# Kernel tuning notes

Measured on AMD Instinct MI355X. Metric: run time of the kernel, lower is better.

## Reference

```python
import jax, jax.numpy as jnp
import numpy as np

EPS = 1e-12


def agnn_layer(x, row, col, num_nodes):
    """AGNN propagation with beta frozen at 1.0 (requires_grad=False in source).
    alpha_ij = softmax_{j in N(i)} ( beta * cos(x_i, x_j) ); out_i = sum_j alpha_ij * x_j.
    row = destination node of each edge (segment id), col = source node.
    """
    xn = x / (jnp.linalg.norm(x, axis=-1, keepdims=True) + EPS)  # unit-norm features
    score = jnp.sum(xn[row] * xn[col], axis=-1)                   # [E] beta=1 * cos sim
    smax = jax.ops.segment_max(score, row, num_segments=num_nodes)
    e = jnp.exp(score - smax[row])                                # stable softmax numerator
    denom = jax.ops.segment_sum(e, row, num_segments=num_nodes)
    alpha = e / jnp.maximum(denom[row], EPS)                      # [E]
    out = jax.ops.segment_sum(alpha[:, None] * x[col], row, num_segments=num_nodes)
    return out


def setup_inputs() -> dict:
    key = jax.random.key(0)
    ks = jax.random.split(key, 8)
    N, E = 100000, 1600000
    IN_DIM, HID, OUT_DIM = 128, 64, 64
    x = jax.random.normal(ks[0], (N, IN_DIM), dtype=jnp.float32)
    edge_row = jnp.sort(jax.random.randint(ks[1], (E,), 0, N))
    edge_col = jax.random.randint(ks[2], (E,), 0, N)
    # Linear params (PyTorch nn.Linear style: y = x @ W.T + b)
    s1 = 1.0 / np.sqrt(IN_DIM)
    W1 = jax.random.uniform(ks[3], (HID, IN_DIM), jnp.float32, -s1, s1)
    b1 = jax.random.uniform(ks[4], (HID,), jnp.float32, -s1, s1)
    s2 = 1.0 / np.sqrt(HID)
    W2 = jax.random.uniform(ks[5], (OUT_DIM, HID), jnp.float32, -s2, s2)
    b2 = jax.random.uniform(ks[6], (OUT_DIM,), jnp.float32, -s2, s2)
    return {"x": x, "edge_row": edge_row, "edge_col": edge_col,
            "W1": W1, "b1": b1, "W2": W2, "b2": b2}


def reference(x, edge_row, edge_col, W1, b1, W2, b2):
    N = x.shape[0]
    h = jax.nn.relu(x @ W1.T + b1)
    for _ in range(4):  # 4 frozen-beta AGNN layers
        h = jax.nn.relu(agnn_layer(h, edge_row, edge_col, N))
    return h @ W2.T + b2
```

## Files before the change

### kernel.cpp

```cpp
#include <hip/hip_runtime.h>


typedef _Float16 h2 __attribute__((ext_vector_type(2)));

union U4H { uint4 u; h2 h[4]; };
union U2H { uint2 u; h2 h[2]; };
union UHI { unsigned u; h2 h; };

#define DEV_INLINE __device__ __forceinline__

DEV_INLINE h2 mkh2(float a, float b) {
    h2 r; r.x = (_Float16)a; r.y = (_Float16)b; return r;
}

__global__ __launch_bounds__(256) void build_rowptr_scan(const int* __restrict__ row,
                                                         int* __restrict__ ptr,
                                                         int N, int E) {
    int e = blockIdx.x * blockDim.x + threadIdx.x;
    if (e >= E) return;
    const int r1 = row[e];
    const int r0 = (e == 0) ? -1 : row[e - 1];
    for (int i = r0 + 1; i <= r1; ++i) ptr[i] = e;
    if (e == E - 1) {
        for (int i = r1 + 1; i <= N; ++i) ptr[i] = E;
    }
}

#define PSEG 1024
__global__ __launch_bounds__(1024) void build_perm_seg(const int* __restrict__ ptr,
                                                       int* __restrict__ perm,
                                                       int N) {
    __shared__ int hist[256];
    __shared__ int tmp[256];
    const int t    = threadIdx.x;
    const int base = blockIdx.x * PSEG;
    const int end  = (base + PSEG < N) ? base + PSEG : N;
    const int cnt  = end - base;

    if (t < 256) hist[t] = 0;
    __syncthreads();

    int d = -1;
    if (t < cnt) {
        d = ptr[base + t + 1] - ptr[base + t];
        if (d > 255) d = 255;
        atomicAdd(&hist[d], 1);
    }
    __syncthreads();

    int h0 = (t < 256) ? hist[t] : 0;
    int* src = hist; int* dst = tmp;
    for (int off = 1; off < 256; off <<= 1) {
        if (t < 256) dst[t] = src[t] + (t >= off ? src[t - off] : 0);
        __syncthreads();
        int* tt = src; src = dst; dst = tt;
    }
    if (t < 256) src[t] -= h0;
    __syncthreads();

    if (t < cnt) {
        int pos = base + atomicAdd(&src[d], 1);
        perm[pos] = base + t;
    }
}

__global__ __launch_bounds__(512) void gemm1_relu(const float* __restrict__ x,
                                                  const float* __restrict__ W1,
                                                  const float* __restrict__ b1,
                                                  unsigned short* __restrict__ xn,
                                                  float* __restrict__ nrm,
                                                  int N) {
    __shared__ __align__(16) float Wt[32 * 64];
    __shared__ __align__(16) float xT[32 * 128];
    const int tid  = threadIdx.x;
    const int tx   = tid & 15;
    const int ty   = tid >> 4;
    const int base = blockIdx.x * 128;

    const float4* W4  = (const float4*)W1;
    const float4* x4p = (const float4*)x;

    const int wO  = tid & 63;
    const int wK4 = tid >> 6;
    const int mA  = tid & 127;
    const int kA  = tid >> 7;
    const int mB  = mA;
    const int kB  = kA + 4;
    const int nodeA = base + mA;

    float4 wv, xa_, xb_;
    wv = W4[wO * 32 + wK4];
    xa_ = make_float4(0.f, 0.f, 0.f, 0.f);
    xb_ = xa_;
    if (nodeA < N) {
        xa_ = x4p[(size_t)nodeA * 32 + kA];
        xb_ = x4p[(size_t)nodeA * 32 + kB];
    }

    float4 b4 = ((const float4*)b1)[tx];
    float4 acc[4];
    acc[0] = b4; acc[1] = b4; acc[2] = b4; acc[3] = b4;

    for (int c = 0; c < 4; ++c) {
        Wt[(4 * wK4 + 0) * 64 + wO] = wv.x;
        Wt[(4 * wK4 + 1) * 64 + wO] = wv.y;
        Wt[(4 * wK4 + 2) * 64 + wO] = wv.z;
        Wt[(4 * wK4 + 3) * 64 + wO] = wv.w;
        xT[(4 * kA + 0) * 128 + mA] = xa_.x;
        xT[(4 * kA + 1) * 128 + mA] = xa_.y;
        xT[(4 * kA + 2) * 128 + mA] = xa_.z;
        xT[(4 * kA + 3) * 128 + mA] = xa_.w;
        xT[(4 * kB + 0) * 128 + mB] = xb_.x;
        xT[(4 * kB + 1) * 128 + mB] = xb_.y;
        xT[(4 * kB + 2) * 128 + mB] = xb_.z;
        xT[(4 * kB + 3) * 128 + mB] = xb_.w;
        __syncthreads();

        if (c < 3) {
            const int ko = (c + 1) * 8;
            wv = W4[wO * 32 + ko + wK4];
            if (nodeA < N) {
                xa_ = x4p[(size_t)nodeA * 32 + ko + kA];
                xb_ = x4p[(size_t)nodeA * 32 + ko + kB];
            }
        }

#pragma unroll 4
        for (int k = 0; k < 32; ++k) {
            const float4 w4 = *(const float4*)&Wt[k * 64 + 4 * tx];
            const float4 xv = *(const float4*)&xT[k * 128 + 4 * ty];
            acc[0].x = fmaf(xv.x, w4.x, acc[0].x);
            acc[0].y = fmaf(xv.x, w4.y, acc[0].y);
            acc[0].z = fmaf(xv.x, w4.z, acc[0].z);
            acc[0].w = fmaf(xv.x, w4.w, acc[0].w);
            acc[1].x = fmaf(xv.y, w4.x, acc[1].x);
            acc[1].y = fmaf(xv.y, w4.y, acc[1].y);
            acc[1].z = fmaf(xv.y, w4.z, acc[1].z);
            acc[1].w = fmaf(xv.y, w4.w, acc[1].w);
            acc[2].x = fmaf(xv.z, w4.x, acc[2].x);
            acc[2].y = fmaf(xv.z, w4.y, acc[2].y);
            acc[2].z = fmaf(xv.z, w4.z, acc[2].z);
            acc[2].w = fmaf(xv.z, w4.w, acc[2].w);
            acc[3].x = fmaf(xv.w, w4.x, acc[3].x);
            acc[3].y = fmaf(xv.w, w4.y, acc[3].y);
            acc[3].z = fmaf(xv.w, w4.z, acc[3].z);
            acc[3].w = fmaf(xv.w, w4.w, acc[3].w);
        }
        if (c < 3) __syncthreads();
    }

#pragma unroll
    for (int mm = 0; mm < 4; ++mm) {
        float4 r = acc[mm];
        r.x = fmaxf(r.x, 0.f); r.y = fmaxf(r.y, 0.f);
        r.z = fmaxf(r.z, 0.f); r.w = fmaxf(r.w, 0.f);
        float s = fmaf(r.x, r.x, fmaf(r.y, r.y, fmaf(r.z, r.z, r.w * r.w)));
        s += __shfl_xor(s, 1, 64);
        s += __shfl_xor(s, 2, 64);
        s += __shfl_xor(s, 4, 64);
        s += __shfl_xor(s, 8, 64);
        const float nn  = sqrtf(s) + 1e-12f;
        const float inv = 1.f / nn;
        int node = base + 4 * ty + mm;
        if (node < N) {
            U2H pk;
            pk.h[0] = mkh2(r.x * inv, r.y * inv);
            pk.h[1] = mkh2(r.z * inv, r.w * inv);
            *(uint2*)&xn[(size_t)node * 64 + 4 * tx] = pk.u;
            if (tx == mm) nrm[node] = nn;
        }
    }
}

__global__ __launch_bounds__(256) void agnn_layer(const uint4* __restrict__ xn4,
                                                  const float* __restrict__ nrm,
                                                  const int* __restrict__ ptr,
                                                  const int* __restrict__ col,
                                                  const int* __restrict__ perm,
                                                  uint4* __restrict__ xo4,
                                                  float* __restrict__ nrmo,
                                                  int N) {
    const int tid  = threadIdx.x;
    const int lane = tid & 63;
    const int g    = (lane >> 3) & 1;
    const int sub  = lane & 7;
    const int slot = blockIdx.x * 16 + (tid >> 4);
    if (slot >= N) return;
    const int i = perm[slot];

    U4H hi_;
    hi_.u = xn4[(unsigned)i * 8u + sub];
    {
        const _Float16 L2E = (_Float16)1.4426950408889634f;
        h2 l2 = {L2E, L2E};
#pragma unroll
        for (int t = 0; t < 4; ++t) hi_.h[t] *= l2;
    }

    const int p0 = ptr[i], p1 = ptr[i + 1];

    float den = 0.f;
    U4H acc;
    acc.h[0] = mkh2(0.f, 0.f); acc.h[1] = mkh2(0.f, 0.f);
    acc.h[2] = mkh2(0.f, 0.f); acc.h[3] = mkh2(0.f, 0.f);

#define EDGE_BODY(VU, NRMJ)                                                  \
    {                                                                        \
        U4H xa; xa.u = (VU);                                                 \
        float s = 0.f;                                                       \
        s = __builtin_amdgcn_fdot2(hi_.h[0], xa.h[0], s, false);             \
        s = __builtin_amdgcn_fdot2(hi_.h[1], xa.h[1], s, false);             \
        s = __builtin_amdgcn_fdot2(hi_.h[2], xa.h[2], s, false);             \
        s = __builtin_amdgcn_fdot2(hi_.h[3], xa.h[3], s, false);             \
        s += __shfl_xor(s, 1, 64);                                           \
        s += __shfl_xor(s, 2, 64);                                           \
        s += __shfl_xor(s, 4, 64);                                           \
        const float p = exp2f(s);                                            \
        den += p;                                                            \
        const _Float16 wh = (_Float16)(p * (NRMJ));                          \
        h2 w2 = {wh, wh};                                                    \
        acc.h[0] += w2 * xa.h[0];                                            \
        acc.h[1] += w2 * xa.h[1];                                            \
        acc.h[2] += w2 * xa.h[2];                                            \
        acc.h[3] += w2 * xa.h[3];                                            \
    }

    int e = p0 + g;
    for (; e + 2 < p1; e += 4) {
        const int ja = col[e];
        const int jb = col[e + 2];
        const uint4 va = xn4[(unsigned)ja * 8u + sub];
        const uint4 vb = xn4[(unsigned)jb * 8u + sub];
        const float na = nrm[ja];
        const float nb = nrm[jb];
        EDGE_BODY(va, na)
        EDGE_BODY(vb, nb)
    }
    if (e < p1) {
        const int j = col[e];
        const uint4 v = xn4[(unsigned)j * 8u + sub];
        const float nj = nrm[j];
        EDGE_BODY(v, nj)
    }
#undef EDGE_BODY

    {
        den += __shfl_xor(den, 8, 64);
#pragma unroll
        for (int t = 0; t < 4; ++t) {
            UHI a; a.h = acc.h[t];
            UHI b; b.u = (unsigned)__shfl_xor((int)a.u, 8, 64);
            acc.h[t] = a.h + b.h;
        }
    }

    const float id = 1.f / fmaxf(den, 1e-12f);
    float o[8];
#pragma unroll
    for (int t = 0; t < 4; ++t) {
        o[2 * t]     = fmaxf((float)acc.h[t].x * id, 0.f);
        o[2 * t + 1] = fmaxf((float)acc.h[t].y * id, 0.f);
    }

    float s2 = 0.f;
#pragma unroll
    for (int t = 0; t < 8; ++t) s2 = fmaf(o[t], o[t], s2);
    s2 += __shfl_xor(s2, 1, 64);
    s2 += __shfl_xor(s2, 2, 64);
    s2 += __shfl_xor(s2, 4, 64);
    const float nn  = sqrtf(s2) + 1e-12f;
    const float inv = 1.f / nn;

    if (g == 0) {
        U4H ov;
        ov.h[0] = mkh2(o[0] * inv, o[1] * inv);
        ov.h[1] = mkh2(o[2] * inv, o[3] * inv);
        ov.h[2] = mkh2(o[4] * inv, o[5] * inv);
        ov.h[3] = mkh2(o[6] * inv, o[7] * inv);
        xo4[(unsigned)i * 8u + sub] = ov.u;
        if (sub == 0) nrmo[i] = nn;
    }
}

__global__ __launch_bounds__(512) void gemm2(const unsigned short* __restrict__ xn,
                                             const float* __restrict__ nrm,
                                             const float* __restrict__ W2,
                                             const float* __restrict__ b2,
                                             float* __restrict__ out,
                                             int N) {
    __shared__ __align__(16) float Wt[64 * 64];
    __shared__ __align__(16) float xT[64 * 128];
    const int tid  = threadIdx.x;
    const int tx   = tid & 15;
    const int ty   = tid >> 4;
    const int base = blockIdx.x * 128;

    {
        const float4* W4 = (const float4*)W2;
#pragma unroll
        for (int it = 0; it < 2; ++it) {
            int idx = tid + it * 512;
            int o = idx & 63, k4 = idx >> 6;
            float4 v = W4[o * 16 + k4];
            Wt[(4 * k4 + 0) * 64 + o] = v.x;
            Wt[(4 * k4 + 1) * 64 + o] = v.y;
            Wt[(4 * k4 + 2) * 64 + o] = v.z;
            Wt[(4 * k4 + 3) * 64 + o] = v.w;
        }
        const uint2* x2 = (const uint2*)xn;
#pragma unroll
        for (int it = 0; it < 4; ++it) {
            int idx = tid + it * 512;
            int mm = idx & 127, k4 = idx >> 7;
            int node = base + mm;
            U2H v; v.u = make_uint2(0u, 0u);
            float nn = 0.f;
            if (node < N) { v.u = x2[(size_t)node * 16 + k4]; nn = nrm[node]; }
            xT[(4 * k4 + 0) * 128 + mm] = (float)v.h[0].x * nn;
            xT[(4 * k4 + 1) * 128 + mm] = (float)v.h[0].y * nn;
            xT[(4 * k4 + 2) * 128 + mm] = (float)v.h[1].x * nn;
            xT[(4 * k4 + 3) * 128 + mm] = (float)v.h[1].y * nn;
        }
    }
    __syncthreads();

    float4 b4 = ((const float4*)b2)[tx];
    float4 acc[4];
    acc[0] = b4; acc[1] = b4; acc[2] = b4; acc[3] = b4;

#pragma unroll 4
    for (int k = 0; k < 64; ++k) {
        const float4 w4 = *(const float4*)&Wt[k * 64 + 4 * tx];
        const float4 xv = *(const float4*)&xT[k * 128 + 4 * ty];
        acc[0].x = fmaf(xv.x, w4.x, acc[0].x);
        acc[0].y = fmaf(xv.x, w4.y, acc[0].y);
        acc[0].z = fmaf(xv.x, w4.z, acc[0].z);
        acc[0].w = fmaf(xv.x, w4.w, acc[0].w);
        acc[1].x = fmaf(xv.y, w4.x, acc[1].x);
        acc[1].y = fmaf(xv.y, w4.y, acc[1].y);
        acc[1].z = fmaf(xv.y, w4.z, acc[1].z);
        acc[1].w = fmaf(xv.y, w4.w, acc[1].w);
        acc[2].x = fmaf(xv.z, w4.x, acc[2].x);
        acc[2].y = fmaf(xv.z, w4.y, acc[2].y);
        acc[2].z = fmaf(xv.z, w4.z, acc[2].z);
        acc[2].w = fmaf(xv.z, w4.w, acc[2].w);
        acc[3].x = fmaf(xv.w, w4.x, acc[3].x);
        acc[3].y = fmaf(xv.w, w4.y, acc[3].y);
        acc[3].z = fmaf(xv.w, w4.z, acc[3].z);
        acc[3].w = fmaf(xv.w, w4.w, acc[3].w);
    }

#pragma unroll
    for (int mm = 0; mm < 4; ++mm) {
        int node = base + 4 * ty + mm;
        if (node < N) *(float4*)&out[(size_t)node * 64 + 4 * tx] = acc[mm];
    }
}

extern "C" void kernel_launch(void* const* d_in, const int* in_sizes, int n_in,
                              void* d_out, int out_size, void* d_ws, size_t ws_size,
                              hipStream_t stream) {
    const float* x   = (const float*)d_in[0];
    const int*   row = (const int*)d_in[1];
    const int*   col = (const int*)d_in[2];
    const float* W1  = (const float*)d_in[3];
    const float* b1  = (const float*)d_in[4];
    const float* W2  = (const float*)d_in[5];
    const float* b2  = (const float*)d_in[6];
    float* out = (float*)d_out;

    const int N = in_sizes[0] / 128;
    const int E = in_sizes[1];

    char* ws = (char*)d_ws;
    size_t off = 0;
    unsigned short* ha = (unsigned short*)(ws + off); off += (size_t)N * 64 * 2;
    unsigned short* hb = (unsigned short*)(ws + off); off += (size_t)N * 64 * 2;
    float* na_  = (float*)(ws + off); off += (size_t)N * sizeof(float);
    float* nb_  = (float*)(ws + off); off += (size_t)N * sizeof(float);
    int*   ptr  = (int*)  (ws + off); off += (size_t)(N + 1) * sizeof(int);
    off = (off + 15) & ~(size_t)15;
    int*   perm = (int*)  (ws + off); off += (size_t)N * sizeof(int);
    (void)ws_size; (void)n_in; (void)out_size;

    build_rowptr_scan<<<(E + 255) / 256, 256, 0, stream>>>(row, ptr, N, E);

    build_perm_seg<<<(N + PSEG - 1) / PSEG, 1024, 0, stream>>>(ptr, perm, N);

    const int nbG = (N + 127) / 128;
    gemm1_relu<<<nbG, 512, 0, stream>>>(x, W1, b1, ha, na_, N);

    const int nb16 = (N + 15) / 16;
    unsigned short* hc = ha; unsigned short* hn = hb;
    float* nc = na_; float* nn = nb_;
    for (int l = 0; l < 4; ++l) {
        agnn_layer<<<nb16, 256, 0, stream>>>((const uint4*)hc, nc, ptr, col, perm,
                                             (uint4*)hn, nn, N);
        unsigned short* t = hc; hc = hn; hn = t;
        float* tf = nc; nc = nn; nn = tf;
    }

    gemm2<<<nbG, 512, 0, stream>>>(hc, nc, W2, b2, out, N);
}
```

Baseline: 301.9 us.

## Stage neighbor rows into LDS via global_load_lds and process edge-per-lane

Restructures the AGNN layer so that each wavefront handles 8 destination nodes. Neighbor feature rows are gathered with global_load_lds directly into a per-wave LDS buffer with XOR swizzling, and each lane then computes one full edge dot product from LDS, which removes the per-edge cross-lane shuffle reductions. Per-lane accumulators are reduced through LDS at the end. In exchange, every node in a wave iterates to the wave's maximum degree, so degree imbalance costs wasted work. Register pressure also rises with the 8-chunk query and accumulator arrays, and each batch waits on a full vmcnt(0) with no overlap between loads and compute.

```diff
diff --git a/kernel.cpp b/kernel.cpp
--- a/kernel.cpp
+++ b/kernel.cpp
@@ -5,7 +5,6 @@
 
 union U4H { uint4 u; h2 h[4]; };
 union U2H { uint2 u; h2 h[2]; };
-union UHI { unsigned u; h2 h; };
 
 #define DEV_INLINE __device__ __forceinline__
 
@@ -179,87 +178,128 @@
                                                   const int* __restrict__ perm,
                                                   uint4* __restrict__ xo4,
                                                   float* __restrict__ nrmo,
-                                                  int N) {
+                                                  int N, int E) {
+    __shared__ uint4 lds_all[4 * 512];
     const int tid  = threadIdx.x;
+    const int wid  = tid >> 6;
     const int lane = tid & 63;
-    const int g    = (lane >> 3) & 1;
-    const int sub  = lane & 7;
-    const int slot = blockIdx.x * 16 + (tid >> 4);
-    if (slot >= N) return;
-    const int i = perm[slot];
-
-    U4H hi_;
-    hi_.u = xn4[(unsigned)i * 8u + sub];
+    const int q    = lane >> 3;
+    const int m    = lane & 7;
+    uint4* W = lds_all + wid * 512;
+
+    const int octet = blockIdx.x * 4 + wid;
+    const int slot  = octet * 8 + q;
+    const bool slotOK = slot < N;
+    const int nid = slotOK ? perm[slot] : 0;
+    const int p0  = ptr[nid];
+    const int p1  = ptr[nid + 1];
+    const int deg = slotOK ? (p1 - p0) : 0;
+
+    int md = deg;
+    md = max(md, __shfl_xor(md, 1, 64));
+    md = max(md, __shfl_xor(md, 2, 64));
+    md = max(md, __shfl_xor(md, 4, 64));
+    md = max(md, __shfl_xor(md, 8, 64));
+    md = max(md, __shfl_xor(md, 16, 64));
+    md = max(md, __shfl_xor(md, 32, 64));
+    const int nbatch = (md + 7) >> 3;
+
+    int p0a[8];
+#pragma unroll
+    for (int k = 0; k < 8; ++k) p0a[k] = __shfl(p0, 8 * k, 64);
+
+    U4H hi[8];
     {
+        const unsigned br = (unsigned)nid * 8u;
+#pragma unroll
+        for (int k = 0; k < 8; ++k) hi[k].u = xn4[br + k];
         const _Float16 L2E = (_Float16)1.4426950408889634f;
         h2 l2 = {L2E, L2E};
 #pragma unroll
-        for (int t = 0; t < 4; ++t) hi_.h[t] *= l2;
-    }
-
-    const int p0 = ptr[i], p1 = ptr[i + 1];
+        for (int k = 0; k < 8; ++k) {
+            hi[k].h[0] *= l2; hi[k].h[1] *= l2;
+            hi[k].h[2] *= l2; hi[k].h[3] *= l2;
+        }
+    }
 
     float den = 0.f;
-    U4H acc;
-    acc.h[0] = mkh2(0.f, 0.f); acc.h[1] = mkh2(0.f, 0.f);
-    acc.h[2] = mkh2(0.f, 0.f); acc.h[3] = mkh2(0.f, 0.f);
-
-#define EDGE_BODY(VU, NRMJ)                                                  \
-    {                                                                        \
-        U4H xa; xa.u = (VU);                                                 \
-        float s = 0.f;                                                       \
-        s = __builtin_amdgcn_fdot2(hi_.h[0], xa.h[0], s, false);             \
-        s = __builtin_amdgcn_fdot2(hi_.h[1], xa.h[1], s, false);             \
-        s = __builtin_amdgcn_fdot2(hi_.h[2], xa.h[2], s, false);             \
-        s = __builtin_amdgcn_fdot2(hi_.h[3], xa.h[3], s, false);             \
-        s += __shfl_xor(s, 1, 64);                                           \
-        s += __shfl_xor(s, 2, 64);                                           \
-        s += __shfl_xor(s, 4, 64);                                           \
-        const float p = exp2f(s);                                            \
-        den += p;                                                            \
-        const _Float16 wh = (_Float16)(p * (NRMJ));                          \
-        h2 w2 = {wh, wh};                                                    \
-        acc.h[0] += w2 * xa.h[0];                                            \
-        acc.h[1] += w2 * xa.h[1];                                            \
-        acc.h[2] += w2 * xa.h[2];                                            \
-        acc.h[3] += w2 * xa.h[3];                                            \
-    }
-
-    int e = p0 + g;
-    for (; e + 2 < p1; e += 4) {
-        const int ja = col[e];
-        const int jb = col[e + 2];
-        const uint4 va = xn4[(unsigned)ja * 8u + sub];
-        const uint4 vb = xn4[(unsigned)jb * 8u + sub];
-        const float na = nrm[ja];
-        const float nb = nrm[jb];
-        EDGE_BODY(va, na)
-        EDGE_BODY(vb, nb)
-    }
-    if (e < p1) {
-        const int j = col[e];
-        const uint4 v = xn4[(unsigned)j * 8u + sub];
-        const float nj = nrm[j];
-        EDGE_BODY(v, nj)
-    }
-#undef EDGE_BODY
-
-    {
-        den += __shfl_xor(den, 8, 64);
-#pragma unroll
-        for (int t = 0; t < 4; ++t) {
-            UHI a; a.h = acc.h[t];
-            UHI b; b.u = (unsigned)__shfl_xor((int)a.u, 8, 64);
-            acc.h[t] = a.h + b.h;
-        }
-    }
+    U4H acc[8];
+#pragma unroll
+    for (int k = 0; k < 8; ++k) {
+        acc[k].h[0] = mkh2(0.f, 0.f); acc[k].h[1] = mkh2(0.f, 0.f);
+        acc[k].h[2] = mkh2(0.f, 0.f); acc[k].h[3] = mkh2(0.f, 0.f);
+    }
+
+    const int rowBase = lane * 8;
+
+    for (int b = 0; b < nbatch; ++b) {
+#pragma unroll
+        for (int k = 0; k < 8; ++k) {
+            int e = p0a[k] + b * 8 + q;
+            e = min(e, E - 1);
+            const int j = col[e];
+            const uint4* src = xn4 + (unsigned)j * 8u + (unsigned)(m ^ q);
+            __builtin_amdgcn_global_load_lds((const unsigned int*)src,
+                                             (unsigned int*)(W + k * 64),
+                                             16, 0, 0);
+        }
+
+        const bool valid = (b * 8 + m) < deg;
+        int eo = p0 + b * 8 + m;
+        eo = min(eo, E - 1);
+        const int jown = col[eo];
+        const float nj = nrm[jown];
+
+        asm volatile("s_waitcnt vmcnt(0)" ::: "memory");
+
+        float s0 = 0.f, s1 = 0.f, s2 = 0.f, s3 = 0.f;
+#pragma unroll
+        for (int k = 0; k < 8; ++k) {
+            U4H rv; rv.u = W[rowBase + (k ^ m)];
+            s0 = __builtin_amdgcn_fdot2(hi[k].h[0], rv.h[0], s0, false);
+            s1 = __builtin_amdgcn_fdot2(hi[k].h[1], rv.h[1], s1, false);
+            s2 = __builtin_amdgcn_fdot2(hi[k].h[2], rv.h[2], s2, false);
+            s3 = __builtin_amdgcn_fdot2(hi[k].h[3], rv.h[3], s3, false);
+        }
+        const float s = (s0 + s1) + (s2 + s3);
+        const float p = valid ? exp2f(s) : 0.f;
+        den += p;
+        const _Float16 wh = (_Float16)(p * nj);
+        h2 w2 = {wh, wh};
+
+#pragma unroll
+        for (int k = 0; k < 8; ++k) {
+            U4H rv; rv.u = W[rowBase + (k ^ m)];
+            acc[k].h[0] += w2 * rv.h[0];
+            acc[k].h[1] += w2 * rv.h[1];
+            acc[k].h[2] += w2 * rv.h[2];
+            acc[k].h[3] += w2 * rv.h[3];
+        }
+    }
+
+#pragma unroll
+    for (int k = 0; k < 8; ++k) W[rowBase + (k ^ m)] = acc[k].u;
+
+    U4H sum;
+    sum.h[0] = mkh2(0.f, 0.f); sum.h[1] = mkh2(0.f, 0.f);
+    sum.h[2] = mkh2(0.f, 0.f); sum.h[3] = mkh2(0.f, 0.f);
+#pragma unroll
+    for (int t = 0; t < 8; ++t) {
+        U4H v; v.u = W[(8 * q + t) * 8 + (m ^ t)];
+        sum.h[0] += v.h[0]; sum.h[1] += v.h[1];
+        sum.h[2] += v.h[2]; sum.h[3] += v.h[3];
+    }
+
+    den += __shfl_xor(den, 1, 64);
+    den += __shfl_xor(den, 2, 64);
+    den += __shfl_xor(den, 4, 64);
 
     const float id = 1.f / fmaxf(den, 1e-12f);
     float o[8];
 #pragma unroll
     for (int t = 0; t < 4; ++t) {
-        o[2 * t]     = fmaxf((float)acc.h[t].x * id, 0.f);
-        o[2 * t + 1] = fmaxf((float)acc.h[t].y * id, 0.f);
+        o[2 * t]     = fmaxf((float)sum.h[t].x * id, 0.f);
+        o[2 * t + 1] = fmaxf((float)sum.h[t].y * id, 0.f);
     }
 
     float s2 = 0.f;
@@ -271,14 +311,14 @@
     const float nn  = sqrtf(s2) + 1e-12f;
     const float inv = 1.f / nn;
 
-    if (g == 0) {
+    if (slotOK) {
         U4H ov;
         ov.h[0] = mkh2(o[0] * inv, o[1] * inv);
         ov.h[1] = mkh2(o[2] * inv, o[3] * inv);
         ov.h[2] = mkh2(o[4] * inv, o[5] * inv);
         ov.h[3] = mkh2(o[6] * inv, o[7] * inv);
-        xo4[(unsigned)i * 8u + sub] = ov.u;
-        if (sub == 0) nrmo[i] = nn;
+        xo4[(unsigned)nid * 8u + m] = ov.u;
+        if (m == 0) nrmo[nid] = nn;
     }
 }
 
@@ -390,12 +430,12 @@
     const int nbG = (N + 127) / 128;
     gemm1_relu<<<nbG, 512, 0, stream>>>(x, W1, b1, ha, na_, N);
 
-    const int nb16 = (N + 15) / 16;
+    const int nb32 = (N + 31) / 32;
     unsigned short* hc = ha; unsigned short* hn = hb;
     float* nc = na_; float* nn = nb_;
     for (int l = 0; l < 4; ++l) {
-        agnn_layer<<<nb16, 256, 0, stream>>>((const uint4*)hc, nc, ptr, col, perm,
-                                             (uint4*)hn, nn, N);
+        agnn_layer<<<nb32, 256, 0, stream>>>((const uint4*)hc, nc, ptr, col, perm,
+                                             (uint4*)hn, nn, N, E);
         unsigned short* t = hc; hc = hn; hn = t;
         float* tf = nc; nc = nn; nn = tf;
     }
```

Measured after the change: 355.5 us. +17.8%, slower.
